# Kernel optimization log

Hardware: AMD Instinct MI355X
Metric: run time of the kernel (lower is better)

## Reference

```python
import jax, jax.numpy as jnp
import numpy as np

B, C, D = 512, 1000, 512
K = 10


def setup_inputs() -> dict:
    key = jax.random.key(0)
    k1, k2, k3, k4, k5 = jax.random.split(key, 5)
    x = jax.random.normal(k1, (B, D), dtype=jnp.float32)
    protos = jax.random.normal(k2, (C, D), dtype=jnp.float32)
    # ex2/ex1 chosen so N*ex2^2 - ex1^2 > 0 (valid sqrt)
    ex2 = jax.random.uniform(k3, (C, D), dtype=jnp.float32) + 1.0
    ex1 = jax.random.uniform(k4, (C, D), dtype=jnp.float32) * 0.1
    cls_num = jax.random.randint(k5, (C,), 1, 100, dtype=jnp.int32)
    proto_label = jnp.arange(C, dtype=jnp.int32)
    return {"x": x, "protos": protos, "ex2": ex2, "ex1": ex1,
            "cls_num": cls_num, "proto_label": proto_label, "k_nearest": K}


def reference(x, protos, ex2, ex1, cls_num, proto_label, k_nearest):
    # rd: per-class, per-feature variance proxy  [C, D]
    N = cls_num[:, None].astype(ex2.dtype)
    rd = jnp.sqrt(N * ex2 ** 2 - ex1 ** 2)
    # softmax over feature dim of (rowmax - rd)
    rd = jax.nn.softmax(jnp.max(rd, axis=1, keepdims=True) - rd, axis=1)
    # weighted squared distances: [B, C, D] -> reduce D -> [B, C]
    diff = x[:, None, :] - protos[None, :, :]
    x_dists = diff ** 2 * rd[None, :, :]
    simi_mat = x_dists.sum(axis=2)  # [B, C]
    # k smallest distances (torch.topk largest=False)
    neg_vals, topk_index = jax.lax.top_k(-simi_mat, k_nearest)
    topk_vals = -neg_vals  # [B, K]
    topk_conf = topk_vals.sum(axis=1, keepdims=True) / topk_vals  # [B, K]
    # pick prototype with max confidence, map through label table
    temp = jnp.argmax(topk_conf, axis=1)  # [B]
    ans_index = jnp.take_along_axis(topk_index, temp[:, None], axis=1)[:, 0]
    predict = proto_label[ans_index]  # [B]
    return predict, topk_conf
```

## Files before the change

### kernel.cpp

```cpp
#include <hip/hip_runtime.h>
#include <math.h>
#include <float.h>

#define B_SZ 512
#define C_SZ 1000
#define D_SZ 512
#define K_TOP 10
#define K2 1024

#define SIMI_OFF 0

#define BM 128
#define BN 16
#define BK 64
#define LDA 72
#define LDB 1032

using f16x8 = __attribute__((ext_vector_type(8))) _Float16;
using f32x4 = __attribute__((ext_vector_type(4))) float;

#if __has_builtin(__builtin_amdgcn_exp2f)
#define FAST_EXP2(x) __builtin_amdgcn_exp2f(x)
#else
#define FAST_EXP2(x) exp2f(x)
#endif
#if __has_builtin(__builtin_amdgcn_sqrtf)
#define FAST_SQRT(x) __builtin_amdgcn_sqrtf(x)
#else
#define FAST_SQRT(x) sqrtf(x)
#endif
#define LOG2E 1.44269504088896340736f

__device__ __forceinline__ void split2(float v, _Float16& h, _Float16& l) {
    h = (_Float16)v;
    l = (_Float16)(v - (float)h);
}

__global__ __launch_bounds__(512, 1) void fused_kernel(const float* __restrict__ x,
                                                       const float* __restrict__ protos,
                                                       const float* __restrict__ ex2,
                                                       const float* __restrict__ ex1,
                                                       const int* __restrict__ cls_num,
                                                       float* __restrict__ simi) {
    __shared__ __align__(16) _Float16 Ah[BM][LDA];
    __shared__ __align__(16) _Float16 Al[BM][LDA];
    __shared__ __align__(16) _Float16 BSh[BN][LDB];
    __shared__ __align__(16) _Float16 BSl[BN][LDB];
    __shared__ float t3s[BN];

    const int tid  = threadIdx.x;
    const int lane = tid & 63;
    const int w    = tid >> 6;
    const int cx = blockIdx.x & 63;
    const int by = blockIdx.x >> 6;
    const int c0 = cx * BN;
    const int b0 = by * BM;
    if (c0 >= C_SZ) return;

    const int srow = tid >> 2;
    const int scol = (tid & 3) * 16;

    auto load_chunk = [&](int ch, float4* dst) {
        const int kx = (ch < 8 ? ch * BK : ch * BK - D_SZ) + scol;
        const float* xp = x + (size_t)(b0 + srow) * D_SZ + kx;
        dst[0] = *(const float4*)(xp);
        dst[1] = *(const float4*)(xp + 4);
        dst[2] = *(const float4*)(xp + 8);
        dst[3] = *(const float4*)(xp + 12);
    };

    float4 cur[4], nxt[4];
    load_chunk(0, cur);

    #pragma unroll
    for (int r = 0; r < 2; r++) {
        const int lc = w * 2 + r;
        const int c  = c0 + lc;
        if (c < C_SZ) {
            const size_t rb = (size_t)c * D_SZ + lane * 8;
            float e2v[8], e1v[8], pv[8];
            *(float4*)&e2v[0] = *(const float4*)(ex2 + rb);
            *(float4*)&e2v[4] = *(const float4*)(ex2 + rb + 4);
            *(float4*)&e1v[0] = *(const float4*)(ex1 + rb);
            *(float4*)&e1v[4] = *(const float4*)(ex1 + rb + 4);
            *(float4*)&pv[0]  = *(const float4*)(protos + rb);
            *(float4*)&pv[4]  = *(const float4*)(protos + rb + 4);
            const float N = (float)cls_num[c];

            float v[8], mn = FLT_MAX;
            #pragma unroll
            for (int k = 0; k < 8; k++) {
                v[k] = FAST_SQRT(N * e2v[k] * e2v[k] - e1v[k] * e1v[k]);
                mn = fminf(mn, v[k]);
            }
            #pragma unroll
            for (int off = 1; off < 64; off <<= 1) mn = fminf(mn, __shfl_xor(mn, off));

            float ev[8], s = 0.f, te = 0.f;
            #pragma unroll
            for (int k = 0; k < 8; k++) {
                ev[k] = FAST_EXP2((mn - v[k]) * LOG2E);
                s += ev[k];
                te = fmaf(ev[k] * pv[k], pv[k], te);
            }
            #pragma unroll
            for (int off = 1; off < 64; off <<= 1) {
                s  += __shfl_xor(s, off);
                te += __shfl_xor(te, off);
            }
            const float inv = 1.0f / s;
            if (lane == 0) t3s[lc] = te * inv;

            f16x8 h1, l1, h2, l2;
            #pragma unroll
            for (int k = 0; k < 8; k++) {
                const float rdv = ev[k] * inv;
                const float w2  = -2.0f * rdv * pv[k];
                _Float16 hh, ll;
                split2(rdv, hh, ll); h1[k] = hh; l1[k] = ll;
                split2(w2,  hh, ll); h2[k] = hh; l2[k] = ll;
            }
            const int d = lane * 8;
            *(f16x8*)&BSh[lc][d]         = h1;
            *(f16x8*)&BSh[lc][D_SZ + d]  = h2;
            *(f16x8*)&BSl[lc][d]         = l1;
            *(f16x8*)&BSl[lc][D_SZ + d]  = l2;
        } else {
            f16x8 z;
            #pragma unroll
            for (int k = 0; k < 8; k++) z[k] = (_Float16)0.f;
            const int d = lane * 8;
            *(f16x8*)&BSh[lc][d]        = z;
            *(f16x8*)&BSh[lc][D_SZ + d] = z;
            *(f16x8*)&BSl[lc][d]        = z;
            *(f16x8*)&BSl[lc][D_SZ + d] = z;
        }
    }
    __syncthreads();

    const int mw = w * 16;
    const int lr = lane & 15;
    const int kg = lane >> 4;

    f32x4 acc;
    #pragma unroll
    for (int r = 0; r < 4; r++) acc[r] = 0.f;

    for (int ch = 0; ch < K2 / BK; ch++) {
        if (ch + 1 < K2 / BK) load_chunk(ch + 1, nxt);

        const bool sq = (ch < 8);
        float av[16];
        *(float4*)&av[0]  = cur[0];
        *(float4*)&av[4]  = cur[1];
        *(float4*)&av[8]  = cur[2];
        *(float4*)&av[12] = cur[3];
        if (sq) {
            #pragma unroll
            for (int k = 0; k < 16; k++) av[k] *= av[k];
        }
        f16x8 ah0, ah1, al0, al1;
        #pragma unroll
        for (int k = 0; k < 8; k++) {
            _Float16 hh, ll;
            split2(av[k], hh, ll);     ah0[k] = hh; al0[k] = ll;
            split2(av[k + 8], hh, ll); ah1[k] = hh; al1[k] = ll;
        }

        __syncthreads();
        *(f16x8*)&Ah[srow][scol]     = ah0;
        *(f16x8*)&Ah[srow][scol + 8] = ah1;
        *(f16x8*)&Al[srow][scol]     = al0;
        *(f16x8*)&Al[srow][scol + 8] = al1;
        __syncthreads();

        #pragma unroll
        for (int sub = 0; sub < 2; sub++) {
            const int kc = sub * 32 + kg * 8;
            const f16x8 fah = *(const f16x8*)&Ah[mw + lr][kc];
            const f16x8 fal = *(const f16x8*)&Al[mw + lr][kc];
            const f16x8 fbh = *(const f16x8*)&BSh[lr][ch * BK + kc];
            const f16x8 fbl = *(const f16x8*)&BSl[lr][ch * BK + kc];
            acc = __builtin_amdgcn_mfma_f32_16x16x32_f16(fal, fbl, acc, 0, 0, 0);
            acc = __builtin_amdgcn_mfma_f32_16x16x32_f16(fah, fbl, acc, 0, 0, 0);
            acc = __builtin_amdgcn_mfma_f32_16x16x32_f16(fal, fbh, acc, 0, 0, 0);
            acc = __builtin_amdgcn_mfma_f32_16x16x32_f16(fah, fbh, acc, 0, 0, 0);
        }

        if (ch + 1 < K2 / BK) {
            cur[0] = nxt[0]; cur[1] = nxt[1];
            cur[2] = nxt[2]; cur[3] = nxt[3];
        }
    }

    const int c = c0 + lr;
    if (c < C_SZ) {
        const float t3v = t3s[lr];
        #pragma unroll
        for (int r = 0; r < 4; r++) {
            const int b = b0 + mw + kg * 4 + r;
            simi[(size_t)b * C_SZ + c] = acc[r] + t3v;
        }
    }
}

__global__ __launch_bounds__(256) void topk_kernel(const float* __restrict__ ws,
                                                   const int* __restrict__ proto_label,
                                                   float* __restrict__ out) {
    const float* simi = ws + SIMI_OFF;
    const int wid = threadIdx.x >> 6;
    const int lane = threadIdx.x & 63;
    const int b = blockIdx.x * 4 + wid;

    float vals[16];
    #pragma unroll
    for (int j = 0; j < 16; j++) {
        const int c = lane + j * 64;
        vals[j] = (c < C_SZ) ? simi[(size_t)b * C_SZ + c] : FLT_MAX;
    }

    float kv[K_TOP];
    int ki[K_TOP];
    for (int t = 0; t < K_TOP; t++) {
        float bv = FLT_MAX;
        int bi = 0x7fffffff;
        #pragma unroll
        for (int j = 0; j < 16; j++) {
            const int c = lane + j * 64;
            if (vals[j] < bv) { bv = vals[j]; bi = c; }
        }
        #pragma unroll
        for (int off = 1; off < 64; off <<= 1) {
            const float ov = __shfl_xor(bv, off);
            const int oi = __shfl_xor(bi, off);
            if (ov < bv || (ov == bv && oi < bi)) { bv = ov; bi = oi; }
        }
        kv[t] = bv;
        ki[t] = bi;
        if ((bi & 63) == lane) vals[bi >> 6] = FLT_MAX;
    }

    if (lane == 0) {
        float S = 0.f;
        #pragma unroll
        for (int t = 0; t < K_TOP; t++) S += kv[t];
        float conf[K_TOP];
        #pragma unroll
        for (int t = 0; t < K_TOP; t++) {
            conf[t] = S / kv[t];
            out[B_SZ + b * K_TOP + t] = conf[t];
        }
        int best = 0;
        for (int t = 1; t < K_TOP; t++)
            if (conf[t] > conf[best]) best = t;
        out[b] = (float)proto_label[ki[best]];
    }
}

extern "C" void kernel_launch(void* const* d_in, const int* in_sizes, int n_in,
                              void* d_out, int out_size, void* d_ws, size_t ws_size,
                              hipStream_t stream) {
    const float* x           = (const float*)d_in[0];
    const float* protos      = (const float*)d_in[1];
    const float* ex2         = (const float*)d_in[2];
    const float* ex1         = (const float*)d_in[3];
    const int*   cls_num     = (const int*)d_in[4];
    const int*   proto_label = (const int*)d_in[5];

    float* ws  = (float*)d_ws;
    float* out = (float*)d_out;

    fused_kernel<<<256, 512, 0, stream>>>(x, protos, ex2, ex1, cls_num,
                                          ws + SIMI_OFF);

    topk_kernel<<<B_SZ / 4, 256, 0, stream>>>(ws, proto_label, out);
}
```

Before: 96.59 us.

## Load A fragments directly from global into MFMA registers, dropping LDS staging

Result: no change. 96.35 us (-0.3%).

```diff
diff --git a/kernel.cpp b/kernel.cpp
--- a/kernel.cpp
+++ b/kernel.cpp
@@ -13,7 +13,6 @@
 #define BM 128
 #define BN 16
 #define BK 64
-#define LDA 72
 #define LDB 1032
 
 using f16x8 = __attribute__((ext_vector_type(8))) _Float16;
@@ -36,14 +35,12 @@
     l = (_Float16)(v - (float)h);
 }
 
-__global__ __launch_bounds__(512, 1) void fused_kernel(const float* __restrict__ x,
+__global__ __launch_bounds__(512, 4) void fused_kernel(const float* __restrict__ x,
                                                        const float* __restrict__ protos,
                                                        const float* __restrict__ ex2,
                                                        const float* __restrict__ ex1,
                                                        const int* __restrict__ cls_num,
                                                        float* __restrict__ simi) {
-    __shared__ __align__(16) _Float16 Ah[BM][LDA];
-    __shared__ __align__(16) _Float16 Al[BM][LDA];
     __shared__ __align__(16) _Float16 BSh[BN][LDB];
     __shared__ __align__(16) _Float16 BSl[BN][LDB];
     __shared__ float t3s[BN];
@@ -57,20 +54,23 @@
     const int b0 = by * BM;
     if (c0 >= C_SZ) return;
 
-    const int srow = tid >> 2;
-    const int scol = (tid & 3) * 16;
-
-    auto load_chunk = [&](int ch, float4* dst) {
-        const int kx = (ch < 8 ? ch * BK : ch * BK - D_SZ) + scol;
-        const float* xp = x + (size_t)(b0 + srow) * D_SZ + kx;
-        dst[0] = *(const float4*)(xp);
-        dst[1] = *(const float4*)(xp + 4);
-        dst[2] = *(const float4*)(xp + 8);
-        dst[3] = *(const float4*)(xp + 12);
+    const int mw = w * 16;
+    const int lr = lane & 15;
+    const int kg = lane >> 4;
+
+    const float* xrow = x + (size_t)(b0 + mw + lr) * D_SZ;
+
+    auto load_a = [&](int ch, float4* d) {
+        const int kx = (ch < 8 ? ch * BK : ch * BK - D_SZ) + kg * 8;
+        const float* xp = xrow + kx;
+        d[0] = *(const float4*)(xp);
+        d[1] = *(const float4*)(xp + 4);
+        d[2] = *(const float4*)(xp + 32);
+        d[3] = *(const float4*)(xp + 36);
     };
 
     float4 cur[4], nxt[4];
-    load_chunk(0, cur);
+    load_a(0, cur);
 
     #pragma unroll
     for (int r = 0; r < 2; r++) {
@@ -138,28 +138,23 @@
     }
     __syncthreads();
 
-    const int mw = w * 16;
-    const int lr = lane & 15;
-    const int kg = lane >> 4;
-
     f32x4 acc;
     #pragma unroll
     for (int r = 0; r < 4; r++) acc[r] = 0.f;
 
     for (int ch = 0; ch < K2 / BK; ch++) {
-        if (ch + 1 < K2 / BK) load_chunk(ch + 1, nxt);
-
-        const bool sq = (ch < 8);
+        if (ch + 1 < K2 / BK) load_a(ch + 1, nxt);
+
         float av[16];
         *(float4*)&av[0]  = cur[0];
         *(float4*)&av[4]  = cur[1];
         *(float4*)&av[8]  = cur[2];
         *(float4*)&av[12] = cur[3];
-        if (sq) {
+        if (ch < 8) {
             #pragma unroll
             for (int k = 0; k < 16; k++) av[k] *= av[k];
         }
-        f16x8 ah0, ah1, al0, al1;
+        f16x8 ah0, al0, ah1, al1;
         #pragma unroll
         for (int k = 0; k < 8; k++) {
             _Float16 hh, ll;
@@ -167,24 +162,22 @@
             split2(av[k + 8], hh, ll); ah1[k] = hh; al1[k] = ll;
         }
 
-        __syncthreads();
-        *(f16x8*)&Ah[srow][scol]     = ah0;
-        *(f16x8*)&Ah[srow][scol + 8] = ah1;
-        *(f16x8*)&Al[srow][scol]     = al0;
-        *(f16x8*)&Al[srow][scol + 8] = al1;
-        __syncthreads();
-
-        #pragma unroll
-        for (int sub = 0; sub < 2; sub++) {
-            const int kc = sub * 32 + kg * 8;
-            const f16x8 fah = *(const f16x8*)&Ah[mw + lr][kc];
-            const f16x8 fal = *(const f16x8*)&Al[mw + lr][kc];
-            const f16x8 fbh = *(const f16x8*)&BSh[lr][ch * BK + kc];
-            const f16x8 fbl = *(const f16x8*)&BSl[lr][ch * BK + kc];
-            acc = __builtin_amdgcn_mfma_f32_16x16x32_f16(fal, fbl, acc, 0, 0, 0);
-            acc = __builtin_amdgcn_mfma_f32_16x16x32_f16(fah, fbl, acc, 0, 0, 0);
-            acc = __builtin_amdgcn_mfma_f32_16x16x32_f16(fal, fbh, acc, 0, 0, 0);
-            acc = __builtin_amdgcn_mfma_f32_16x16x32_f16(fah, fbh, acc, 0, 0, 0);
+        const int kb = ch * BK + kg * 8;
+        {
+            const f16x8 fbh = *(const f16x8*)&BSh[lr][kb];
+            const f16x8 fbl = *(const f16x8*)&BSl[lr][kb];
+            acc = __builtin_amdgcn_mfma_f32_16x16x32_f16(al0, fbl, acc, 0, 0, 0);
+            acc = __builtin_amdgcn_mfma_f32_16x16x32_f16(ah0, fbl, acc, 0, 0, 0);
+            acc = __builtin_amdgcn_mfma_f32_16x16x32_f16(al0, fbh, acc, 0, 0, 0);
+            acc = __builtin_amdgcn_mfma_f32_16x16x32_f16(ah0, fbh, acc, 0, 0, 0);
+        }
+        {
+            const f16x8 fbh = *(const f16x8*)&BSh[lr][kb + 32];
+            const f16x8 fbl = *(const f16x8*)&BSl[lr][kb + 32];
+            acc = __builtin_amdgcn_mfma_f32_16x16x32_f16(al1, fbl, acc, 0, 0, 0);
+            acc = __builtin_amdgcn_mfma_f32_16x16x32_f16(ah1, fbl, acc, 0, 0, 0);
+            acc = __builtin_amdgcn_mfma_f32_16x16x32_f16(al1, fbh, acc, 0, 0, 0);
+            acc = __builtin_amdgcn_mfma_f32_16x16x32_f16(ah1, fbh, acc, 0, 0, 0);
         }
 
         if (ch + 1 < K2 / BK) {
```
